# Optimization experiments

Hardware: AMD Instinct MI355X
Metric: run time of the kernel (lower is better)

Reference implementation:

```python
import jax, jax.numpy as jnp
import numpy as np

T, B, H1 = 256, 8, 512
U, H2 = 64, 512
V = 128


def setup_inputs() -> dict:
    key = jax.random.key(0)
    k1, k2, k3, k4, k5, k6 = jax.random.split(key, 6)
    f = jax.random.normal(k1, (T, B, H1), dtype=jnp.float32)
    g = jax.random.normal(k2, (B, U, H2), dtype=jnp.float32)
    f_lens = jax.random.randint(k3, (B,), 1, T + 1)
    g_lens = jax.random.randint(k4, (B,), 1, U + 1)
    W = jax.random.normal(k5, (H1 + H2, V), dtype=jnp.float32) * (1.0 / np.sqrt(H1 + H2))
    b = jax.random.normal(k6, (V,), dtype=jnp.float32) * 0.01
    return {"f": f, "f_lens": f_lens, "g": g, "g_lens": g_lens, "W": W, "b": b}


def reference(f, f_lens, g, g_lens, W, b):
    # Original: f [T,B,H1] -> [B,T,1,H1] expand, g [B,U,H2] -> [B,1,U,H2] expand,
    # concat on last dim -> [B,T,U,H1+H2], then Linear over last dim.
    # Linear(concat) == f @ W[:H1] + g @ W[H1:] + b, broadcast-summed -- same math,
    # without materializing the [B,T,U,H1+H2] intermediate.
    Wf, Wg = W[:H1], W[H1:]
    pf = jnp.einsum('tbh,hv->btv', f, Wf)          # [B,T,V]
    pg = jnp.einsum('buh,hv->buv', g, Wg)          # [B,U,V]
    h = pf[:, :, None, :] + pg[:, None, :, :] + b  # [B,T,U,V]
    return h, f_lens
```

## Files before the change

### kernel.cpp

```cpp
#include <hip/hip_runtime.h>
#include <hip/hip_bf16.h>


typedef float  f32x4  __attribute__((ext_vector_type(4)));
typedef short  bh8    __attribute__((ext_vector_type(8)));

__device__ __forceinline__ unsigned short f2bf(float x) {
    unsigned u = __float_as_uint(x);
    unsigned r = u + 0x7FFFu + ((u >> 16) & 1u);
    return (unsigned short)(r >> 16);
}

__global__ __launch_bounds__(256) void wtrans2(const float* __restrict__ W,
                                               short* __restrict__ Wt) {
    int gid = blockIdx.x * 256 + threadIdx.x;
    int v   = gid & 127;
    int h0  = (gid >> 7) * 16;
    short tmp[16];
#pragma unroll
    for (int i = 0; i < 16; ++i)
        tmp[i] = (short)f2bf(W[(h0 + i) * 128 + v]);
    bh8* dst = reinterpret_cast<bh8*>(Wt + v * 1024 + h0);
    dst[0] = *reinterpret_cast<bh8*>(&tmp[0]);
    dst[1] = *reinterpret_cast<bh8*>(&tmp[8]);
}

__global__ __launch_bounds__(256) void proj2(const float* __restrict__ F,
                                             const float* __restrict__ G,
                                             const short* __restrict__ Wt,
                                             float* __restrict__ P) {
    __shared__ float red[4][16][128];

    const int tid  = threadIdx.x;
    const int w    = tid >> 6;
    const int lane = tid & 63;
    const int l15  = lane & 15;
    const int cc   = lane >> 4;
    const int rowBase = blockIdx.x * 16;
    const bool isF = rowBase < 2048;
    const int koff = isF ? 0 : 512;

    const int r = rowBase + l15;
    const float* arow;
    if (isF) { int b = r >> 8, t = r & 255; arow = F + ((t << 3) + b) * 512; }
    else     { arow = G + (r - 2048) * 512; }

    f32x4 acc[8] = {};

#pragma unroll
    for (int kk = 0; kk < 4; ++kk) {
        const int k0 = w * 128 + kk * 32 + cc * 8;
        f32x4 a0 = *reinterpret_cast<const f32x4*>(arow + k0);
        f32x4 a1 = *reinterpret_cast<const f32x4*>(arow + k0 + 4);
        bh8 av;
        av[0] = (short)f2bf(a0[0]); av[1] = (short)f2bf(a0[1]);
        av[2] = (short)f2bf(a0[2]); av[3] = (short)f2bf(a0[3]);
        av[4] = (short)f2bf(a1[0]); av[5] = (short)f2bf(a1[1]);
        av[6] = (short)f2bf(a1[2]); av[7] = (short)f2bf(a1[3]);
#pragma unroll
        for (int j = 0; j < 8; ++j) {
            const short* bsrc = Wt + (j * 16 + l15) * 1024 + koff + k0;
            bh8 bv = *reinterpret_cast<const bh8*>(bsrc);
            acc[j] = __builtin_amdgcn_mfma_f32_16x16x32_bf16(av, bv, acc[j], 0, 0, 0);
        }
    }

#pragma unroll
    for (int j = 0; j < 8; ++j)
#pragma unroll
        for (int q = 0; q < 4; ++q)
            red[w][cc * 4 + q][j * 16 + l15] = acc[j][q];
    __syncthreads();

    const int row = tid >> 4, colq = tid & 15;
    f32x4 s0 = {}, s1 = {};
#pragma unroll
    for (int ww = 0; ww < 4; ++ww) {
        s0 += *reinterpret_cast<const f32x4*>(&red[ww][row][colq * 8]);
        s1 += *reinterpret_cast<const f32x4*>(&red[ww][row][colq * 8 + 4]);
    }
    float* pdst = P + (rowBase + row) * 128 + colq * 8;
    *reinterpret_cast<f32x4*>(pdst)     = s0;
    *reinterpret_cast<f32x4*>(pdst + 4) = s1;
}

__global__ __launch_bounds__(256) void bcast(const float* __restrict__ P,
                                             const float* __restrict__ bias,
                                             const int* __restrict__ f_lens,
                                             float* __restrict__ out,
                                             int lens_off) {
    const int r   = blockIdx.x;
    const int tid = threadIdx.x;
    const int b   = r >> 8;
    const int vq  = tid & 31;
    const int u0  = tid >> 5;

    f32x4 pf = *reinterpret_cast<const f32x4*>(P + r * 128 + vq * 4);
    f32x4 bi = *reinterpret_cast<const f32x4*>(bias + vq * 4);
    pf += bi;

    const float* pg = P + (2048 + b * 64) * 128;
    float* ob = out + (size_t)r * 8192;

#pragma unroll
    for (int i = 0; i < 8; ++i) {
        int u = u0 * 8 + i;
        f32x4 v = *reinterpret_cast<const f32x4*>(pg + u * 128 + vq * 4);
        v += pf;
        *reinterpret_cast<f32x4*>(ob + u * 128 + vq * 4) = v;
    }

    if (r == 0 && tid < 8) out[lens_off + tid] = (float)f_lens[tid];
}

extern "C" void kernel_launch(void* const* d_in, const int* in_sizes, int n_in,
                              void* d_out, int out_size, void* d_ws, size_t ws_size,
                              hipStream_t stream) {
    const float* f      = (const float*)d_in[0];
    const int*   f_lens = (const int*)  d_in[1];
    const float* g      = (const float*)d_in[2];
    const float* W      = (const float*)d_in[4];
    const float* bias   = (const float*)d_in[5];
    float* out = (float*)d_out;

    short* Wt = (short*)d_ws;
    float* P  = (float*)((char*)d_ws + 262144);

    wtrans2<<<dim3(32),   dim3(256), 0, stream>>>(W, Wt);
    proj2  <<<dim3(160),  dim3(256), 0, stream>>>(f, g, Wt, P);
    bcast  <<<dim3(2048), dim3(256), 0, stream>>>(P, bias, f_lens, out, out_size - 8);
}
```

Before: 28.91 us.

## Fuse f-projection into broadcast kernel and merge weight prep with g-projection

Cuts the pipeline from three launches to two. The first kernel now runs the weight transpose and the g projection side by side, with the g projection reading fp32 W directly and converting it to bf16 in registers. The second kernel computes the f projection for 8 timesteps per block with MFMA and writes the broadcast output directly, dropping the P round trip through global memory for f. The trade-offs are half-wasted MFMA rows (only 8 of 16 rows used), uncoalesced strided W reads in the g path, and a much heavier per-block store loop across only 256 blocks.

After: 28.16 us. -2.6%, faster.

```diff
diff --git a/kernel.cpp b/kernel.cpp
--- a/kernel.cpp
+++ b/kernel.cpp
@@ -2,51 +2,38 @@
 #include <hip/hip_bf16.h>
 
 
-typedef float  f32x4  __attribute__((ext_vector_type(4)));
-typedef short  bh8    __attribute__((ext_vector_type(8)));
+typedef float  f32x4 __attribute__((ext_vector_type(4)));
+typedef short  bh8   __attribute__((ext_vector_type(8)));
 
 __device__ __forceinline__ unsigned short f2bf(float x) {
     unsigned u = __float_as_uint(x);
-    unsigned r = u + 0x7FFFu + ((u >> 16) & 1u);
-    return (unsigned short)(r >> 16);
+    return (unsigned short)((u + 0x7FFFu + ((u >> 16) & 1u)) >> 16);
 }
 
-__global__ __launch_bounds__(256) void wtrans2(const float* __restrict__ W,
-                                               short* __restrict__ Wt) {
-    int gid = blockIdx.x * 256 + threadIdx.x;
-    int v   = gid & 127;
-    int h0  = (gid >> 7) * 16;
-    short tmp[16];
+__global__ __launch_bounds__(256) void prep(const float* __restrict__ W,
+                                            const float* __restrict__ G,
+                                            short* __restrict__ Wt,
+                                            float* __restrict__ Pg) {
+    __shared__ float red[4][16][128];
+    const int tid = threadIdx.x;
+
+    if (blockIdx.x < 32) {
+        int gid = blockIdx.x * 256 + tid;
+        int v = gid & 127, h0 = (gid >> 7) * 16;
+        short tmp[16];
 #pragma unroll
-    for (int i = 0; i < 16; ++i)
-        tmp[i] = (short)f2bf(W[(h0 + i) * 128 + v]);
-    bh8* dst = reinterpret_cast<bh8*>(Wt + v * 1024 + h0);
-    dst[0] = *reinterpret_cast<bh8*>(&tmp[0]);
-    dst[1] = *reinterpret_cast<bh8*>(&tmp[8]);
-}
+        for (int i = 0; i < 16; ++i) tmp[i] = (short)f2bf(W[(h0 + i) * 128 + v]);
+        bh8* dst = reinterpret_cast<bh8*>(Wt + v * 1024 + h0);
+        dst[0] = *reinterpret_cast<bh8*>(&tmp[0]);
+        dst[1] = *reinterpret_cast<bh8*>(&tmp[8]);
+        return;
+    }
 
-__global__ __launch_bounds__(256) void proj2(const float* __restrict__ F,
-                                             const float* __restrict__ G,
-                                             const short* __restrict__ Wt,
-                                             float* __restrict__ P) {
-    __shared__ float red[4][16][128];
-
-    const int tid  = threadIdx.x;
-    const int w    = tid >> 6;
-    const int lane = tid & 63;
-    const int l15  = lane & 15;
-    const int cc   = lane >> 4;
-    const int rowBase = blockIdx.x * 16;
-    const bool isF = rowBase < 2048;
-    const int koff = isF ? 0 : 512;
-
-    const int r = rowBase + l15;
-    const float* arow;
-    if (isF) { int b = r >> 8, t = r & 255; arow = F + ((t << 3) + b) * 512; }
-    else     { arow = G + (r - 2048) * 512; }
+    const int rowBase = (blockIdx.x - 32) * 16;
+    const int w = tid >> 6, lane = tid & 63, l15 = lane & 15, cc = lane >> 4;
+    const float* arow = G + (rowBase + l15) * 512;
 
     f32x4 acc[8] = {};
-
 #pragma unroll
     for (int kk = 0; kk < 4; ++kk) {
         const int k0 = w * 128 + kk * 32 + cc * 8;
@@ -59,12 +46,13 @@
         av[6] = (short)f2bf(a1[2]); av[7] = (short)f2bf(a1[3]);
 #pragma unroll
         for (int j = 0; j < 8; ++j) {
-            const short* bsrc = Wt + (j * 16 + l15) * 1024 + koff + k0;
-            bh8 bv = *reinterpret_cast<const bh8*>(bsrc);
+            const float* wsrc = W + (512 + k0) * 128 + (j * 16 + l15);
+            bh8 bv;
+#pragma unroll
+            for (int i = 0; i < 8; ++i) bv[i] = (short)f2bf(wsrc[i * 128]);
             acc[j] = __builtin_amdgcn_mfma_f32_16x16x32_bf16(av, bv, acc[j], 0, 0, 0);
         }
     }
-
 #pragma unroll
     for (int j = 0; j < 8; ++j)
 #pragma unroll
@@ -79,38 +67,77 @@
         s0 += *reinterpret_cast<const f32x4*>(&red[ww][row][colq * 8]);
         s1 += *reinterpret_cast<const f32x4*>(&red[ww][row][colq * 8 + 4]);
     }
-    float* pdst = P + (rowBase + row) * 128 + colq * 8;
+    float* pdst = Pg + (rowBase + row) * 128 + colq * 8;
     *reinterpret_cast<f32x4*>(pdst)     = s0;
     *reinterpret_cast<f32x4*>(pdst + 4) = s1;
 }
 
-__global__ __launch_bounds__(256) void bcast(const float* __restrict__ P,
-                                             const float* __restrict__ bias,
-                                             const int* __restrict__ f_lens,
-                                             float* __restrict__ out,
-                                             int lens_off) {
-    const int r   = blockIdx.x;
+__global__ __launch_bounds__(256) void fuse(const float* __restrict__ F,
+                                            const short* __restrict__ Wt,
+                                            const float* __restrict__ Pg,
+                                            const float* __restrict__ bias,
+                                            const int* __restrict__ f_lens,
+                                            float* __restrict__ out, int lens_off) {
+    __shared__ float pfred[4][8][128];
+
     const int tid = threadIdx.x;
-    const int b   = r >> 8;
-    const int vq  = tid & 31;
-    const int u0  = tid >> 5;
+    const int b = blockIdx.x >> 5, t0 = (blockIdx.x & 31) * 8;
+    const int w = tid >> 6, lane = tid & 63, l15 = lane & 15, cc = lane >> 4;
 
-    f32x4 pf = *reinterpret_cast<const f32x4*>(P + r * 128 + vq * 4);
-    f32x4 bi = *reinterpret_cast<const f32x4*>(bias + vq * 4);
-    pf += bi;
+    const int t = t0 + (l15 & 7);
+    const float* arow = F + (t * 8 + b) * 512;
 
-    const float* pg = P + (2048 + b * 64) * 128;
-    float* ob = out + (size_t)r * 8192;
+    f32x4 acc[8] = {};
+#pragma unroll
+    for (int kk = 0; kk < 4; ++kk) {
+        const int k0 = w * 128 + kk * 32 + cc * 8;
+        f32x4 a0 = *reinterpret_cast<const f32x4*>(arow + k0);
+        f32x4 a1 = *reinterpret_cast<const f32x4*>(arow + k0 + 4);
+        bh8 av;
+        av[0] = (short)f2bf(a0[0]); av[1] = (short)f2bf(a0[1]);
+        av[2] = (short)f2bf(a0[2]); av[3] = (short)f2bf(a0[3]);
+        av[4] = (short)f2bf(a1[0]); av[5] = (short)f2bf(a1[1]);
+        av[6] = (short)f2bf(a1[2]); av[7] = (short)f2bf(a1[3]);
+#pragma unroll
+        for (int j = 0; j < 8; ++j) {
+            bh8 bv = *reinterpret_cast<const bh8*>(Wt + (j * 16 + l15) * 1024 + k0);
+            acc[j] = __builtin_amdgcn_mfma_f32_16x16x32_bf16(av, bv, acc[j], 0, 0, 0);
+        }
+    }
+    if (cc < 2) {
+#pragma unroll
+        for (int j = 0; j < 8; ++j)
+#pragma unroll
+            for (int q = 0; q < 4; ++q)
+                pfred[w][cc * 4 + q][j * 16 + l15] = acc[j][q];
+    }
+    __syncthreads();
 
+    const int vq = tid & 31, ug = tid >> 5;
+    const f32x4 bi = *reinterpret_cast<const f32x4*>(bias + vq * 4);
+
+    f32x4 pfv[8], pgv[8];
 #pragma unroll
-    for (int i = 0; i < 8; ++i) {
-        int u = u0 * 8 + i;
-        f32x4 v = *reinterpret_cast<const f32x4*>(pg + u * 128 + vq * 4);
-        v += pf;
-        *reinterpret_cast<f32x4*>(ob + u * 128 + vq * 4) = v;
+    for (int t2 = 0; t2 < 8; ++t2) {
+        f32x4 s = *reinterpret_cast<const f32x4*>(&pfred[0][t2][vq * 4]);
+        s += *reinterpret_cast<const f32x4*>(&pfred[1][t2][vq * 4]);
+        s += *reinterpret_cast<const f32x4*>(&pfred[2][t2][vq * 4]);
+        s += *reinterpret_cast<const f32x4*>(&pfred[3][t2][vq * 4]);
+        pfv[t2] = s + bi;
     }
+#pragma unroll
+    for (int ui = 0; ui < 8; ++ui)
+        pgv[ui] = *reinterpret_cast<const f32x4*>(Pg + (b * 64 + ui * 8 + ug) * 128 + vq * 4);
 
-    if (r == 0 && tid < 8) out[lens_off + tid] = (float)f_lens[tid];
+    float* ob = out + (size_t)(b * 256 + t0) * 8192;
+#pragma unroll
+    for (int t2 = 0; t2 < 8; ++t2)
+#pragma unroll
+        for (int ui = 0; ui < 8; ++ui)
+            *reinterpret_cast<f32x4*>(ob + (t2 * 64 + ui * 8 + ug) * 128 + vq * 4)
+                = pfv[t2] + pgv[ui];
+
+    if (blockIdx.x == 0 && tid < 8) out[lens_off + tid] = (float)f_lens[tid];
 }
 
 extern "C" void kernel_launch(void* const* d_in, const int* in_sizes, int n_in,
@@ -123,10 +150,9 @@
     const float* bias   = (const float*)d_in[5];
     float* out = (float*)d_out;
 
-    short* Wt = (short*)d_ws;
-    float* P  = (float*)((char*)d_ws + 262144);
+    float* Pg = (float*)d_ws;
+    short* Wt = (short*)((char*)d_ws + 262144);
 
-    wtrans2<<<dim3(32),   dim3(256), 0, stream>>>(W, Wt);
-    proj2  <<<dim3(160),  dim3(256), 0, stream>>>(f, g, Wt, P);
-    bcast  <<<dim3(2048), dim3(256), 0, stream>>>(P, bias, f_lens, out, out_size - 8);
+    prep<<<dim3(64),  dim3(256), 0, stream>>>(W, g, Wt, Pg);
+    fuse<<<dim3(256), dim3(256), 0, stream>>>(f, Wt, Pg, bias, f_lens, out, out_size - 8);
 }
```

## Fuse weight bf16 conversion into projection and halve rows per block

Applied to the files above, without the earlier changes.

Drops the separate W transpose/convert kernel. The projection kernel now reads fp32 W directly with strided loads and converts it to bf16 on the fly. Each block now handles 8 rows instead of 16, doubling the grid to 320 blocks, so the MFMA lanes for rows 8-15 duplicate work whose results are thrown away. This removes one kernel launch and the Wt round trip, at the cost of uncoalesced, redundant W loads and half-wasted MFMA throughput.

Measured after the change: 26.36 us. 8.8% less time.

```diff
diff --git a/kernel.cpp b/kernel.cpp
--- a/kernel.cpp
+++ b/kernel.cpp
@@ -2,51 +2,31 @@
 #include <hip/hip_bf16.h>
 
 
-typedef float  f32x4  __attribute__((ext_vector_type(4)));
-typedef short  bh8    __attribute__((ext_vector_type(8)));
+typedef float  f32x4 __attribute__((ext_vector_type(4)));
+typedef short  bh8   __attribute__((ext_vector_type(8)));
 
 __device__ __forceinline__ unsigned short f2bf(float x) {
     unsigned u = __float_as_uint(x);
-    unsigned r = u + 0x7FFFu + ((u >> 16) & 1u);
-    return (unsigned short)(r >> 16);
+    return (unsigned short)((u + 0x7FFFu + ((u >> 16) & 1u)) >> 16);
 }
 
-__global__ __launch_bounds__(256) void wtrans2(const float* __restrict__ W,
-                                               short* __restrict__ Wt) {
-    int gid = blockIdx.x * 256 + threadIdx.x;
-    int v   = gid & 127;
-    int h0  = (gid >> 7) * 16;
-    short tmp[16];
-#pragma unroll
-    for (int i = 0; i < 16; ++i)
-        tmp[i] = (short)f2bf(W[(h0 + i) * 128 + v]);
-    bh8* dst = reinterpret_cast<bh8*>(Wt + v * 1024 + h0);
-    dst[0] = *reinterpret_cast<bh8*>(&tmp[0]);
-    dst[1] = *reinterpret_cast<bh8*>(&tmp[8]);
-}
+__global__ __launch_bounds__(256) void proj3(const float* __restrict__ F,
+                                             const float* __restrict__ G,
+                                             const float* __restrict__ W,
+                                             float* __restrict__ P) {
+    __shared__ float sred[4][8][128];
 
-__global__ __launch_bounds__(256) void proj2(const float* __restrict__ F,
-                                             const float* __restrict__ G,
-                                             const short* __restrict__ Wt,
-                                             float* __restrict__ P) {
-    __shared__ float red[4][16][128];
+    const int tid = threadIdx.x;
+    const int rows8 = blockIdx.x * 8;
+    const bool isF = rows8 < 2048;
+    const int koff = isF ? 0 : 512;
+    const int w = tid >> 6, lane = tid & 63, l15 = lane & 15, cc = lane >> 4;
 
-    const int tid  = threadIdx.x;
-    const int w    = tid >> 6;
-    const int lane = tid & 63;
-    const int l15  = lane & 15;
-    const int cc   = lane >> 4;
-    const int rowBase = blockIdx.x * 16;
-    const bool isF = rowBase < 2048;
-    const int koff = isF ? 0 : 512;
-
-    const int r = rowBase + l15;
-    const float* arow;
-    if (isF) { int b = r >> 8, t = r & 255; arow = F + ((t << 3) + b) * 512; }
-    else     { arow = G + (r - 2048) * 512; }
+    const int rr = rows8 + (l15 & 7);
+    const float* arow = isF ? F + (((rr & 255) << 3) + (rr >> 8)) * 512
+                            : G + (rr - 2048) * 512;
 
     f32x4 acc[8] = {};
-
 #pragma unroll
     for (int kk = 0; kk < 4; ++kk) {
         const int k0 = w * 128 + kk * 32 + cc * 8;
@@ -59,29 +39,28 @@
         av[6] = (short)f2bf(a1[2]); av[7] = (short)f2bf(a1[3]);
 #pragma unroll
         for (int j = 0; j < 8; ++j) {
-            const short* bsrc = Wt + (j * 16 + l15) * 1024 + koff + k0;
-            bh8 bv = *reinterpret_cast<const bh8*>(bsrc);
+            const float* wsrc = W + (koff + k0) * 128 + (j * 16 + l15);
+            bh8 bv;
+#pragma unroll
+            for (int i = 0; i < 8; ++i) bv[i] = (short)f2bf(wsrc[i * 128]);
             acc[j] = __builtin_amdgcn_mfma_f32_16x16x32_bf16(av, bv, acc[j], 0, 0, 0);
         }
     }
-
+    if (cc < 2) {
 #pragma unroll
-    for (int j = 0; j < 8; ++j)
+        for (int j = 0; j < 8; ++j)
 #pragma unroll
-        for (int q = 0; q < 4; ++q)
-            red[w][cc * 4 + q][j * 16 + l15] = acc[j][q];
+            for (int q = 0; q < 4; ++q)
+                sred[w][cc * 4 + q][j * 16 + l15] = acc[j][q];
+    }
     __syncthreads();
 
-    const int row = tid >> 4, colq = tid & 15;
-    f32x4 s0 = {}, s1 = {};
-#pragma unroll
-    for (int ww = 0; ww < 4; ++ww) {
-        s0 += *reinterpret_cast<const f32x4*>(&red[ww][row][colq * 8]);
-        s1 += *reinterpret_cast<const f32x4*>(&red[ww][row][colq * 8 + 4]);
-    }
-    float* pdst = P + (rowBase + row) * 128 + colq * 8;
-    *reinterpret_cast<f32x4*>(pdst)     = s0;
-    *reinterpret_cast<f32x4*>(pdst + 4) = s1;
+    const int row = tid >> 5, colq = tid & 31;
+    f32x4 s = *reinterpret_cast<const f32x4*>(&sred[0][row][colq * 4]);
+    s += *reinterpret_cast<const f32x4*>(&sred[1][row][colq * 4]);
+    s += *reinterpret_cast<const f32x4*>(&sred[2][row][colq * 4]);
+    s += *reinterpret_cast<const f32x4*>(&sred[3][row][colq * 4]);
+    *reinterpret_cast<f32x4*>(P + (rows8 + row) * 128 + colq * 4) = s;
 }
 
 __global__ __launch_bounds__(256) void bcast(const float* __restrict__ P,
@@ -123,10 +102,8 @@
     const float* bias   = (const float*)d_in[5];
     float* out = (float*)d_out;
 
-    short* Wt = (short*)d_ws;
-    float* P  = (float*)((char*)d_ws + 262144);
+    float* P = (float*)d_ws;
 
-    wtrans2<<<dim3(32),   dim3(256), 0, stream>>>(W, Wt);
-    proj2  <<<dim3(160),  dim3(256), 0, stream>>>(f, g, Wt, P);
-    bcast  <<<dim3(2048), dim3(256), 0, stream>>>(P, bias, f_lens, out, out_size - 8);
+    proj3<<<dim3(320),  dim3(256), 0, stream>>>(f, g, W, P);
+    bcast<<<dim3(2048), dim3(256), 0, stream>>>(P, bias, f_lens, out, out_size - 8);
 }
```
